# Performance work log

Hardware: AMD Instinct MI355X
Metric: run time of the kernel (lower is better)

Reference implementation:

```python
import jax, jax.numpy as jnp
import numpy as np

TOTAL_LABELS = 21
TOTAL_POS_BBOXES = 64


def _make_boxes(key, batch, n):
    # valid [y1,x1,y2,x2] boxes in [0,1]
    k1, k2 = jax.random.split(key)
    tl = jax.random.uniform(k1, (batch, n, 2)) * 0.7          # y1, x1
    wh = jax.random.uniform(k2, (batch, n, 2)) * 0.3 + 0.01   # h, w
    br = jnp.minimum(tl + wh, 1.0)                            # y2, x2
    return jnp.concatenate([tl, br], axis=-1).astype(jnp.float32)


def setup_inputs() -> dict:
    key = jax.random.key(0)
    k1, k2, k3 = jax.random.split(key, 3)
    batch, n_roi, n_gt = 32, 2000, 100
    roi_bboxes = _make_boxes(k1, batch, n_roi)
    gt_boxes = _make_boxes(k2, batch, n_gt)
    gt_labels = jax.random.randint(k3, (batch, n_gt), 0, TOTAL_LABELS, dtype=jnp.int32)
    return {"roi_bboxes": roi_bboxes, "gt_boxes": gt_boxes, "gt_labels": gt_labels}


def generate_iou_map(bboxes, gt_boxes):
    # bboxes: (b, n, 4), gt_boxes: (b, m, 4) -> iou: (b, n, m)
    by1, bx1, by2, bx2 = jnp.split(bboxes, 4, axis=-1)        # each (b, n, 1)
    gy1, gx1, gy2, gx2 = jnp.split(gt_boxes, 4, axis=-1)      # each (b, m, 1)
    gt_area = jnp.squeeze((gy2 - gy1) * (gx2 - gx1), axis=-1)  # (b, m)
    bb_area = jnp.squeeze((by2 - by1) * (bx2 - bx1), axis=-1)  # (b, n)
    x_top = jnp.maximum(bx1, jnp.swapaxes(gx1, 1, 2))
    y_top = jnp.maximum(by1, jnp.swapaxes(gy1, 1, 2))
    x_bot = jnp.minimum(bx2, jnp.swapaxes(gx2, 1, 2))
    y_bot = jnp.minimum(by2, jnp.swapaxes(gy2, 1, 2))
    inter = jnp.maximum(x_bot - x_top, 0.0) * jnp.maximum(y_bot - y_top, 0.0)  # (b, n, m)
    union = bb_area[:, :, None] + gt_area[:, None, :] - inter
    return inter / union


def get_deltas_from_bboxes(bboxes, gt_boxes):
    bw = bboxes[..., 3] - bboxes[..., 1]
    bh = bboxes[..., 2] - bboxes[..., 0]
    bcx = bboxes[..., 1] + 0.5 * bw
    bcy = bboxes[..., 0] + 0.5 * bh
    gw = gt_boxes[..., 3] - gt_boxes[..., 1]
    gh = gt_boxes[..., 2] - gt_boxes[..., 0]
    gcx = gt_boxes[..., 1] + 0.5 * gw
    gcy = gt_boxes[..., 0] + 0.5 * gh
    bw = jnp.where(bw == 0, 1e-3, bw)
    bh = jnp.where(bh == 0, 1e-3, bh)
    dx = jnp.where(gw == 0, 0.0, (gcx - bcx) / bw)
    dy = jnp.where(gh == 0, 0.0, (gcy - bcy) / bh)
    dw = jnp.where(gw == 0, 0.0, jnp.log(jnp.where(gw == 0, 1.0, gw / bw)))
    dh = jnp.where(gh == 0, 0.0, jnp.log(jnp.where(gh == 0, 1.0, gh / bh)))
    return jnp.stack([dy, dx, dh, dw], axis=-1)


def reference(roi_bboxes, gt_boxes, gt_labels):
    batch, n_roi = roi_bboxes.shape[0], roi_bboxes.shape[1]
    iou_map = generate_iou_map(roi_bboxes, gt_boxes)                 # (b, n, m)
    max_idx = jnp.argmax(iou_map, axis=2).astype(jnp.int32)          # (b, n)
    merged = jnp.max(iou_map, axis=2)                                # (b, n)
    order = jnp.argsort(-merged, axis=1)                             # descending
    rank = jnp.argsort(order, axis=1)                                # rank of each roi
    pos_mask = rank < TOTAL_POS_BBOXES                               # (b, n)
    gt_boxes_map = jnp.take_along_axis(gt_boxes, max_idx[..., None], axis=1)   # (b, n, 4)
    expanded_gt_boxes = jnp.where(pos_mask[..., None], gt_boxes_map, 0.0)
    gt_labels_map = jnp.take_along_axis(gt_labels, max_idx, axis=1)  # (b, n)
    expanded_gt_labels = jnp.where(pos_mask, gt_labels_map, 0)
    deltas = get_deltas_from_bboxes(roi_bboxes, expanded_gt_boxes)   # (b, n, 4)
    labels = jax.nn.one_hot(expanded_gt_labels, TOTAL_LABELS, dtype=deltas.dtype)  # (b, n, L)
    # per-class delta expansion: (b, n, L, 1) * (b, n, 1, 4) -> (b, n*L, 4)
    roi_bbox_deltas = (labels[..., None] * deltas[:, :, None, :]).reshape(
        batch, n_roi * TOTAL_LABELS, 4)
    return (jax.lax.stop_gradient(roi_bbox_deltas), jax.lax.stop_gradient(labels))
```

## Files before the change

### kernel.cpp

```cpp
#include <hip/hip_runtime.h>

#define BATCH 32
#define NROI  2000
#define NGT   100
#define NLBL  21
#define NPOS  64

__global__ __launch_bounds__(256) void iou_max_kernel(
    const float4* __restrict__ roi, const float4* __restrict__ gt,
    unsigned long long* __restrict__ keys, int* __restrict__ maxidx) {
  __shared__ float4 sgt[NGT];
  const int b = blockIdx.y;
  const int r = blockIdx.x * 256 + threadIdx.x;
  if (threadIdx.x < NGT) sgt[threadIdx.x] = gt[b * NGT + threadIdx.x];
  __syncthreads();
  if (r >= NROI) return;
  float4 rb = roi[b * NROI + r];
  float bb_area = __fmul_rn(__fsub_rn(rb.z, rb.x), __fsub_rn(rb.w, rb.y));
  float best = -1.0f;
  int bi = 0;
#pragma unroll 4
  for (int m = 0; m < NGT; ++m) {
    float4 g = sgt[m];
    float ga = __fmul_rn(__fsub_rn(g.z, g.x), __fsub_rn(g.w, g.y));
    float xt = fmaxf(rb.y, g.y);
    float yt = fmaxf(rb.x, g.x);
    float xb = fminf(rb.w, g.w);
    float yb = fminf(rb.z, g.z);
    float iw = fmaxf(__fsub_rn(xb, xt), 0.0f);
    float ih = fmaxf(__fsub_rn(yb, yt), 0.0f);
    float inter = __fmul_rn(iw, ih);
    float uni = __fsub_rn(__fadd_rn(bb_area, ga), inter);
    float iou = __fdiv_rn(inter, uni);
    if (iou > best) { best = iou; bi = m; }
  }
  unsigned int fb = __float_as_uint(best);
  keys[b * NROI + r] =
      ((unsigned long long)fb << 16) | (unsigned long long)(0xFFFFu - (unsigned)r);
  maxidx[b * NROI + r] = bi;
}

__global__ __launch_bounds__(256) void select_delta_kernel(
    const unsigned long long* __restrict__ keys, const int* __restrict__ maxidx,
    const float4* __restrict__ roi, const float4* __restrict__ gt,
    const int* __restrict__ gtlab,
    float4* __restrict__ dlt, int* __restrict__ lab) {
  const int b = blockIdx.x;
  const int t = threadIdx.x;
  unsigned long long k[8];
#pragma unroll
  for (int j = 0; j < 8; ++j) {
    int i = t + j * 256;
    k[j] = (i < NROI) ? keys[b * NROI + i] : 0ull;
  }
  __shared__ int scnt[4];
  unsigned long long lo = 0, hi = 0x3F800000FFFFull;
  while (lo < hi) {
    unsigned long long mid = lo + ((hi - lo) >> 1);
    int c = 0;
#pragma unroll
    for (int j = 0; j < 8; ++j) c += (k[j] > mid) ? 1 : 0;
#pragma unroll
    for (int off = 32; off > 0; off >>= 1) c += __shfl_down(c, off, 64);
    if ((t & 63) == 0) scnt[t >> 6] = c;
    __syncthreads();
    int tot = scnt[0] + scnt[1] + scnt[2] + scnt[3];
    if (tot <= NPOS - 1) hi = mid; else lo = mid + 1;
    __syncthreads();
  }
  const unsigned long long k64 = lo;
#pragma unroll
  for (int j = 0; j < 8; ++j) {
    int i = t + j * 256;
    if (i >= NROI) continue;
    int ridx = b * NROI + i;
    float4 d = make_float4(0.f, 0.f, 0.f, 0.f);
    int lb = 0;
    if (k[j] >= k64) {
      int mi = maxidx[ridx];
      float4 g = gt[b * NGT + mi];
      float4 rb = roi[ridx];
      float bw = rb.w - rb.y, bh = rb.z - rb.x;
      float bcx = rb.y + 0.5f * bw, bcy = rb.x + 0.5f * bh;
      float gw = g.w - g.y, gh = g.z - g.x;
      float gcx = g.y + 0.5f * gw, gcy = g.x + 0.5f * gh;
      if (bw == 0.f) bw = 1e-3f;
      if (bh == 0.f) bh = 1e-3f;
      float dx  = (gw == 0.f) ? 0.f : (gcx - bcx) / bw;
      float dy  = (gh == 0.f) ? 0.f : (gcy - bcy) / bh;
      float dwv = (gw == 0.f) ? 0.f : logf(gw / bw);
      float dhv = (gh == 0.f) ? 0.f : logf(gh / bh);
      d = make_float4(dy, dx, dhv, dwv);
      lb = gtlab[b * NGT + mi];
    }
    dlt[ridx] = d;
    lab[ridx] = lb;
  }
}

__global__ __launch_bounds__(256) void write_out_kernel(
    const float4* __restrict__ dlt, const int* __restrict__ lab,
    float4* __restrict__ out) {
  const int ND4 = BATCH * NROI * NLBL;
  const int NL4 = (BATCH * NROI * NLBL) / 4;
  int i = blockIdx.x * 256 + threadIdx.x;
  if (i < ND4) {
    int b = i / (NROI * NLBL);
    int rem = i - b * (NROI * NLBL);
    int r = rem / NLBL;
    int cls = rem - r * NLBL;
    int ridx = b * NROI + r;
    float4 v = make_float4(0.f, 0.f, 0.f, 0.f);
    if (cls == lab[ridx]) v = dlt[ridx];
    out[i] = v;
  } else if (i < ND4 + NL4) {
    int i2 = i - ND4;
    int e = i2 * 4;
    float v[4];
#pragma unroll
    for (int kk = 0; kk < 4; ++kk) {
      int ei = e + kk;
      int b = ei / (NROI * NLBL);
      int rem = ei - b * (NROI * NLBL);
      int r = rem / NLBL;
      int cls = rem - r * NLBL;
      v[kk] = (cls == lab[b * NROI + r]) ? 1.0f : 0.0f;
    }
    out[i] = make_float4(v[0], v[1], v[2], v[3]);
  }
}

extern "C" void kernel_launch(void* const* d_in, const int* in_sizes, int n_in,
                              void* d_out, int out_size, void* d_ws, size_t ws_size,
                              hipStream_t stream) {
  const float* roi = (const float*)d_in[0];
  const float* gt  = (const float*)d_in[1];
  const int* gtlab = (const int*)d_in[2];

  char* ws = (char*)d_ws;
  unsigned long long* keys = (unsigned long long*)ws;
  int*    maxidx = (int*)(ws + 512000);
  float4* dlt    = (float4*)(ws + 768000);
  int*    lab    = (int*)(ws + 1792000);

  iou_max_kernel<<<dim3(8, BATCH), 256, 0, stream>>>(
      (const float4*)roi, (const float4*)gt, keys, maxidx);
  select_delta_kernel<<<dim3(BATCH), 256, 0, stream>>>(
      keys, maxidx, (const float4*)roi, (const float4*)gt, gtlab, dlt, lab);
  const int total4 = BATCH * NROI * NLBL + (BATCH * NROI * NLBL) / 4;
  write_out_kernel<<<dim3((total4 + 255) / 256), 256, 0, stream>>>(
      dlt, lab, (float4*)d_out);
}
```

Baseline: 107.6 us.

## Radix-select top-k threshold, move delta math to writer, use nontemporal stores

The 64-bit binary search for the top-64 threshold (about 48 iterations, each with two barriers) is replaced by a 6-pass 8-bit radix select using a shared-memory histogram and a prefix scan. GT box areas are precomputed once in shared memory instead of being recomputed inside the IoU loop. Delta computation moves from the select kernel into the output writer, which now computes deltas only for the matching class. Output stores become nontemporal to avoid polluting the cache with the large write-only output. The radix select adds atomics and more complex scan logic.

```diff
diff --git a/kernel.cpp b/kernel.cpp
--- a/kernel.cpp
+++ b/kernel.cpp
@@ -6,13 +6,25 @@
 #define NLBL  21
 #define NPOS  64
 
+typedef float nfloat4 __attribute__((ext_vector_type(4)));
+
+__device__ __forceinline__ void nt_store(const float4& v, float4* p) {
+  nfloat4 nv = {v.x, v.y, v.z, v.w};
+  __builtin_nontemporal_store(nv, (nfloat4*)p);
+}
+
 __global__ __launch_bounds__(256) void iou_max_kernel(
     const float4* __restrict__ roi, const float4* __restrict__ gt,
     unsigned long long* __restrict__ keys, int* __restrict__ maxidx) {
   __shared__ float4 sgt[NGT];
+  __shared__ float sga[NGT];
   const int b = blockIdx.y;
   const int r = blockIdx.x * 256 + threadIdx.x;
-  if (threadIdx.x < NGT) sgt[threadIdx.x] = gt[b * NGT + threadIdx.x];
+  if (threadIdx.x < NGT) {
+    float4 g = gt[b * NGT + threadIdx.x];
+    sgt[threadIdx.x] = g;
+    sga[threadIdx.x] = __fmul_rn(__fsub_rn(g.z, g.x), __fsub_rn(g.w, g.y));
+  }
   __syncthreads();
   if (r >= NROI) return;
   float4 rb = roi[b * NROI + r];
@@ -22,7 +34,6 @@
 #pragma unroll 4
   for (int m = 0; m < NGT; ++m) {
     float4 g = sgt[m];
-    float ga = __fmul_rn(__fsub_rn(g.z, g.x), __fsub_rn(g.w, g.y));
     float xt = fmaxf(rb.y, g.y);
     float yt = fmaxf(rb.x, g.x);
     float xb = fminf(rb.w, g.w);
@@ -30,7 +41,7 @@
     float iw = fmaxf(__fsub_rn(xb, xt), 0.0f);
     float ih = fmaxf(__fsub_rn(yb, yt), 0.0f);
     float inter = __fmul_rn(iw, ih);
-    float uni = __fsub_rn(__fadd_rn(bb_area, ga), inter);
+    float uni = __fsub_rn(__fadd_rn(bb_area, sga[m]), inter);
     float iou = __fdiv_rn(inter, uni);
     if (iou > best) { best = iou; bi = m; }
   }
@@ -40,11 +51,10 @@
   maxidx[b * NROI + r] = bi;
 }
 
-__global__ __launch_bounds__(256) void select_delta_kernel(
+__global__ __launch_bounds__(256) void select_kernel(
     const unsigned long long* __restrict__ keys, const int* __restrict__ maxidx,
-    const float4* __restrict__ roi, const float4* __restrict__ gt,
-    const int* __restrict__ gtlab,
-    float4* __restrict__ dlt, int* __restrict__ lab) {
+    const float4* __restrict__ gt, const int* __restrict__ gtlab,
+    float4* __restrict__ egt, int* __restrict__ lab) {
   const int b = blockIdx.x;
   const int t = threadIdx.x;
   unsigned long long k[8];
@@ -53,32 +63,75 @@
     int i = t + j * 256;
     k[j] = (i < NROI) ? keys[b * NROI + i] : 0ull;
   }
-  __shared__ int scnt[4];
-  unsigned long long lo = 0, hi = 0x3F800000FFFFull;
-  while (lo < hi) {
-    unsigned long long mid = lo + ((hi - lo) >> 1);
-    int c = 0;
+  __shared__ int hist[256];
+  __shared__ int wtot[4];
+  __shared__ int sbin, sneed;
+  unsigned long long prefix = 0;
+  int need = NPOS;
+  const int lane = t & 63;
 #pragma unroll
-    for (int j = 0; j < 8; ++j) c += (k[j] > mid) ? 1 : 0;
+  for (int p = 0; p < 6; ++p) {
+    const int shift = 40 - 8 * p;
+    hist[t] = 0;
+    __syncthreads();
+    const unsigned long long hmask = ~((1ull << (shift + 8)) - 1);
 #pragma unroll
-    for (int off = 32; off > 0; off >>= 1) c += __shfl_down(c, off, 64);
-    if ((t & 63) == 0) scnt[t >> 6] = c;
+    for (int j = 0; j < 8; ++j) {
+      if ((k[j] & hmask) == prefix)
+        atomicAdd(&hist[(int)((k[j] >> shift) & 255)], 1);
+    }
     __syncthreads();
-    int tot = scnt[0] + scnt[1] + scnt[2] + scnt[3];
-    if (tot <= NPOS - 1) hi = mid; else lo = mid + 1;
+    int v = hist[t];
+    int S = v;
+#pragma unroll
+    for (int off = 1; off < 64; off <<= 1) {
+      int u = __shfl_down(S, off, 64);
+      if (lane + off < 64) S += u;
+    }
+    if (lane == 0) wtot[t >> 6] = S;
     __syncthreads();
+    int w = t >> 6;
+#pragma unroll
+    for (int w2 = 1; w2 < 4; ++w2)
+      if (w2 > w) S += wtot[w2];
+    if (S >= need && (S - v) < need) { sbin = t; sneed = need - (S - v); }
+    __syncthreads();
+    prefix |= ((unsigned long long)sbin) << shift;
+    need = sneed;
   }
-  const unsigned long long k64 = lo;
+  const unsigned long long k64 = prefix;
 #pragma unroll
   for (int j = 0; j < 8; ++j) {
     int i = t + j * 256;
     if (i >= NROI) continue;
     int ridx = b * NROI + i;
-    float4 d = make_float4(0.f, 0.f, 0.f, 0.f);
+    float4 g = make_float4(0.f, 0.f, 0.f, 0.f);
     int lb = 0;
     if (k[j] >= k64) {
       int mi = maxidx[ridx];
-      float4 g = gt[b * NGT + mi];
+      g = gt[b * NGT + mi];
+      lb = gtlab[b * NGT + mi];
+    }
+    egt[ridx] = g;
+    lab[ridx] = lb;
+  }
+}
+
+__global__ __launch_bounds__(256) void write_out_kernel(
+    const float4* __restrict__ roi, const float4* __restrict__ egt,
+    const int* __restrict__ lab, float4* __restrict__ out) {
+  const int ND4 = BATCH * NROI * NLBL;
+  const int NL4 = (BATCH * NROI * NLBL) / 4;
+  int i = blockIdx.x * 256 + threadIdx.x;
+  if (i < ND4) {
+    int b = i / (NROI * NLBL);
+    int rem = i - b * (NROI * NLBL);
+    int r = rem / NLBL;
+    int cls = rem - r * NLBL;
+    int ridx = b * NROI + r;
+    float4 v = make_float4(0.f, 0.f, 0.f, 0.f);
+    if (cls == lab[ridx]) {
+      float4 g = egt[ridx];
       float4 rb = roi[ridx];
       float bw = rb.w - rb.y, bh = rb.z - rb.x;
       float bcx = rb.y + 0.5f * bw, bcy = rb.x + 0.5f * bh;
@@ -90,29 +143,9 @@
       float dy  = (gh == 0.f) ? 0.f : (gcy - bcy) / bh;
       float dwv = (gw == 0.f) ? 0.f : logf(gw / bw);
       float dhv = (gh == 0.f) ? 0.f : logf(gh / bh);
-      d = make_float4(dy, dx, dhv, dwv);
-      lb = gtlab[b * NGT + mi];
+      v = make_float4(dy, dx, dhv, dwv);
     }
-    dlt[ridx] = d;
-    lab[ridx] = lb;
-  }
-}
-
-__global__ __launch_bounds__(256) void write_out_kernel(
-    const float4* __restrict__ dlt, const int* __restrict__ lab,
-    float4* __restrict__ out) {
-  const int ND4 = BATCH * NROI * NLBL;
-  const int NL4 = (BATCH * NROI * NLBL) / 4;
-  int i = blockIdx.x * 256 + threadIdx.x;
-  if (i < ND4) {
-    int b = i / (NROI * NLBL);
-    int rem = i - b * (NROI * NLBL);
-    int r = rem / NLBL;
-    int cls = rem - r * NLBL;
-    int ridx = b * NROI + r;
-    float4 v = make_float4(0.f, 0.f, 0.f, 0.f);
-    if (cls == lab[ridx]) v = dlt[ridx];
-    out[i] = v;
+    nt_store(v, &out[i]);
   } else if (i < ND4 + NL4) {
     int i2 = i - ND4;
     int e = i2 * 4;
@@ -126,7 +159,8 @@
       int cls = rem - r * NLBL;
       v[kk] = (cls == lab[b * NROI + r]) ? 1.0f : 0.0f;
     }
-    out[i] = make_float4(v[0], v[1], v[2], v[3]);
+    float4 vv = make_float4(v[0], v[1], v[2], v[3]);
+    nt_store(vv, &out[i]);
   }
 }
 
@@ -140,14 +174,14 @@
   char* ws = (char*)d_ws;
   unsigned long long* keys = (unsigned long long*)ws;
   int*    maxidx = (int*)(ws + 512000);
-  float4* dlt    = (float4*)(ws + 768000);
+  float4* egt    = (float4*)(ws + 768000);
   int*    lab    = (int*)(ws + 1792000);
 
   iou_max_kernel<<<dim3(8, BATCH), 256, 0, stream>>>(
       (const float4*)roi, (const float4*)gt, keys, maxidx);
-  select_delta_kernel<<<dim3(BATCH), 256, 0, stream>>>(
-      keys, maxidx, (const float4*)roi, (const float4*)gt, gtlab, dlt, lab);
+  select_kernel<<<dim3(BATCH), 256, 0, stream>>>(
+      keys, maxidx, (const float4*)gt, gtlab, egt, lab);
   const int total4 = BATCH * NROI * NLBL + (BATCH * NROI * NLBL) / 4;
   write_out_kernel<<<dim3((total4 + 255) / 256), 256, 0, stream>>>(
-      dlt, lab, (float4*)d_out);
+      (const float4*)roi, egt, lab, (float4*)d_out);
 }
```

Result: faster. 88.26 us (-18.0%).
